# Optimization experiments

Hardware: AMD Instinct MI355X
Metric: run time of the kernel (lower is better)

The kernel has to match this reference:

```python
import jax, jax.numpy as jnp
import numpy as np

B, S, D = 4, 512, 256

def setup_inputs() -> dict:
    key = jax.random.key(0)
    ks = jax.random.split(key, 32)
    def w(k, shape, s=0.05):
        return jax.random.normal(k, shape, dtype=jnp.float32) * s
    inp = {
        "img": jax.random.normal(ks[0], (B, S, D), dtype=jnp.float32),
        "audio": jax.random.normal(ks[1], (B, S, D), dtype=jnp.float32),
        "common": jax.random.normal(ks[2], (B, S, D), dtype=jnp.float32),
    }
    names = ["qv", "qa", "kv", "ka", "cc", "w5", "w6", "w7", "w8"]
    for i, n in enumerate(names):
        inp[n + "_w"] = w(ks[3 + 2 * i], (D, D))   # stored [in, out]
        inp[n + "_b"] = w(ks[4 + 2 * i], (D,))
    inp["bil_w"] = w(ks[25], (D, D, D))            # Bilinear weight [out, in1, in2]
    inp["t_o"] = jnp.ones((), dtype=jnp.float32)
    return inp


def reference(img, audio, common,
              qv_w, qv_b, qa_w, qa_b, kv_w, kv_b, ka_w, ka_b, cc_w, cc_b,
              w5_w, w5_b, w6_w, w6_b, w7_w, w7_b, w8_w, w8_b,
              bil_w, t_o):
    dim_k = qv_w.shape[1]
    norm_fact = 1.0 / jnp.sqrt(jnp.asarray(dim_k, dtype=jnp.float32))

    lin = lambda x, w, b: x @ w + b
    # NOTE: faithful to source - softmax first, THEN scaled by norm_fact.
    attn = lambda q, k: jax.nn.softmax(jnp.einsum('bsd,btd->bst', q, k), axis=-1) * norm_fact

    W_q_v = lin(img, qv_w, qv_b)
    W_q_a = lin(audio, qa_w, qa_b)
    w_k_a = lin(audio, ka_w, ka_b)
    W_k_v = lin(img, kv_w, kv_b)
    C_c = lin(common, cc_w, cc_b)

    atten_vv = attn(W_q_v, W_k_v)
    atten_vc = attn(W_q_v, C_c)
    atten_aa = attn(W_q_a, w_k_a)
    atten_ac = attn(W_q_a, C_c)

    vc_common = jnp.einsum('bst,btd->bsd', atten_vc, common)
    ac_common = jnp.einsum('bst,btd->bsd', atten_ac, common)

    common_feat_v = (1.0 + lin(vc_common, w5_w, w5_b)) * jnp.einsum('bst,btd->bsd', atten_vv, img) + lin(vc_common, w6_w, w6_b)
    common_feat_a = (1.0 + lin(ac_common, w7_w, w7_b)) * jnp.einsum('bst,btd->bsd', atten_aa, audio) + lin(ac_common, w8_w, w8_b)

    # Bilinear: out[b,s,k] = v[b,s,:] @ W[k] @ a[b,s,:]
    atten_m = jnp.einsum('bsi,kij,bsj->bsk', common_feat_v, bil_w, common_feat_a)
    j_o = jax.nn.sigmoid(atten_m)
    Z_k_o = t_o * j_o * img + (1.0 - j_o) * audio
    return (Z_k_o + img, Z_k_o + audio)
```

## Files before the change

### kernel.cpp

```cpp
#include <hip/hip_runtime.h>
#include <hip/hip_bf16.h>

typedef unsigned short ushortT;
typedef __bf16 bf16x8 __attribute__((ext_vector_type(8)));
typedef float f32x4 __attribute__((ext_vector_type(4)));
typedef ushortT ush8 __attribute__((ext_vector_type(8)));
typedef ushortT ush4 __attribute__((ext_vector_type(4)));

#define MFMA16(a, b, c) __builtin_amdgcn_mfma_f32_16x16x32_bf16((a), (b), (c), 0, 0, 0)

__device__ __forceinline__ ushortT f2b(float f) {
  __hip_bfloat16 h = __float2bfloat16(f);
  return __builtin_bit_cast(ushortT, h);
}
__device__ __forceinline__ float b2f(ushortT u) {
  __hip_bfloat16 h = __builtin_bit_cast(__hip_bfloat16, u);
  return __bfloat162float(h);
}

__device__ __forceinline__ void async16(const void* g, void* l) {
  __builtin_amdgcn_global_load_lds((const __attribute__((address_space(1))) unsigned int*)g,
                                   (__attribute__((address_space(3))) unsigned int*)l, 16, 0, 0);
}

#define ACT_E 524288
#define WD_E  65536

#define OFF_ACT16   0u
#define OFF_ACTT16  3145728u
#define OFF_W16T    6291456u
#define OFF_PROJ16  7471104u
#define OFF_P16     12713984u
#define OFF_VC16    21102592u
#define OFF_AC16    22151168u
#define OFF_PVV32   23199744u
#define OFF_PVA32   25296896u
#define OFF_PART    0u
#define OFF_BIL16   33554432u
#define OFF_CFV16   67108864u
#define OFF_CFA16   68157440u

__global__ void k_cvt_acts(const float* __restrict__ img, const float* __restrict__ aud,
                           const float* __restrict__ com, ushortT* __restrict__ dst) {
  int i4 = blockIdx.x * 256 + threadIdx.x;
#pragma unroll
  for (int q = 0; q < 4; q++) {
    int idx4 = i4 + q * 98304;
    int flat = idx4 * 4;
    const float* src;
    int off;
    if (flat < 524288)        { src = img; off = flat; }
    else if (flat < 1048576)  { src = aud; off = flat - 524288; }
    else                      { src = com; off = flat - 1048576; }
    float4 v = *(const float4*)(src + off);
    ush4 u = { f2b(v.x), f2b(v.y), f2b(v.z), f2b(v.w) };
    *(ush4*)(dst + idx4 * 4) = u;
  }
}

__global__ void k_cvt_bil(const float* __restrict__ bil, ushortT* __restrict__ dst) {
  int i4 = blockIdx.x * 256 + threadIdx.x;
#pragma unroll
  for (int q = 0; q < 8; q++) {
    int idx4 = i4 + q * 524288;
    float4 v = *(const float4*)(bil + idx4 * 4);
    ush4 u = { f2b(v.x), f2b(v.y), f2b(v.z), f2b(v.w) };
    *(ush4*)(dst + idx4 * 4) = u;
  }
}

__global__ void k_transpose(const float* __restrict__ img, const float* __restrict__ aud,
                            const float* __restrict__ com,
                            const float* w0, const float* w1, const float* w2,
                            const float* w3, const float* w4, const float* w5,
                            const float* w6, const float* w7, const float* w8,
                            ushortT* __restrict__ actT, ushortT* __restrict__ wT) {
  __shared__ ushortT tl[64][72];
  int tid = threadIdx.x;
  int bx = blockIdx.x;
  const float* src;
  ushortT* dst;
  int R, C, r0, c0;
  if (bx < 384) {
    int inst = bx >> 5, tile = bx & 31;
    int act = inst >> 2, bb = inst & 3;
    src = (act == 0 ? img : (act == 1 ? aud : com)) + bb * 131072;
    dst = actT + act * 524288 + bb * 131072;
    R = 512; C = 256;
    r0 = (tile >> 2) * 64; c0 = (tile & 3) * 64;
  } else {
    int bw = bx - 384;
    int w = bw >> 4, tile = bw & 15;
    const float* s;
    switch (w) {
      case 0: s = w0; break; case 1: s = w1; break; case 2: s = w2; break;
      case 3: s = w3; break; case 4: s = w4; break; case 5: s = w5; break;
      case 6: s = w6; break; case 7: s = w7; break; default: s = w8; break;
    }
    src = s;
    dst = wT + w * 65536;
    R = 256; C = 256;
    r0 = (tile >> 2) * 64; c0 = (tile & 3) * 64;
  }
#pragma unroll
  for (int q = 0; q < 4; q++) {
    int rr = q * 16 + (tid >> 4);
    int cs = (tid & 15) * 4;
    float4 v = *(const float4*)(src + (r0 + rr) * C + c0 + cs);
    tl[rr][cs + 0] = f2b(v.x);
    tl[rr][cs + 1] = f2b(v.y);
    tl[rr][cs + 2] = f2b(v.z);
    tl[rr][cs + 3] = f2b(v.w);
  }
  __syncthreads();
#pragma unroll
  for (int q = 0; q < 4; q++) {
    int cc = q * 16 + (tid >> 4);
    int rs = (tid & 15) * 4;
    ush4 u = { tl[rs + 0][cc], tl[rs + 1][cc], tl[rs + 2][cc], tl[rs + 3][cc] };
    *(ush4*)(dst + (c0 + cc) * R + r0 + rs) = u;
  }
}

__global__ __launch_bounds__(512) void k_linear5(
    const ushortT* __restrict__ act16, const ushortT* __restrict__ wT,
    const float* __restrict__ b0, const float* __restrict__ b1,
    const float* __restrict__ b2, const float* __restrict__ b3,
    const float* __restrict__ b4, ushortT* __restrict__ proj16) {
  __shared__ ushortT Al[4][32][8];
  __shared__ ushortT Bl[4][256][8];
  const int tid = threadIdx.x, l = tid & 63, w = tid >> 6;
  const int bx = blockIdx.x;
  const int op = bx >> 6, sblk = bx & 63;
  const int s0 = sblk * 32;
  const int xsel = (op == 4) ? 2 : (op & 1);
  const ushortT* X = act16 + xsel * ACT_E;
  const ushortT* W = wT + op * WD_E;
  const float* bias = op == 0 ? b0 : op == 1 ? b1 : op == 2 ? b2 : op == 3 ? b3 : b4;
  ushortT* out = proj16 + op * ACT_E;

  f32x4 acc[2][2] = {};
  ush8 ra, rb[2];
  int a_row = tid >> 2, a_seg = tid & 3;

  auto sload = [&](int k0) {
    if (tid < 128) ra = *(const ush8*)(X + (s0 + a_row) * 256 + k0 + a_seg * 8);
#pragma unroll
    for (int q = 0; q < 2; q++) {
      int slot = tid + q * 512;
      rb[q] = *(const ush8*)(W + (slot >> 2) * 256 + k0 + (slot & 3) * 8);
    }
  };
  auto swrite = [&]() {
    if (tid < 128) *(ush8*)(&Al[a_seg][a_row][0]) = ra;
#pragma unroll
    for (int q = 0; q < 2; q++) {
      int slot = tid + q * 512;
      *(ush8*)(&Bl[slot & 3][slot >> 2][0]) = rb[q];
    }
  };

  sload(0); swrite(); __syncthreads();
  for (int s = 0; s < 8; s++) {
    if (s < 7) sload((s + 1) * 32);
    int ks = l >> 4;
    bf16x8 a[2], bb[2];
#pragma unroll
    for (int m = 0; m < 2; m++) a[m] = *(const bf16x8*)(&Al[ks][m * 16 + (l & 15)][0]);
#pragma unroll
    for (int n = 0; n < 2; n++) bb[n] = *(const bf16x8*)(&Bl[ks][w * 32 + n * 16 + (l & 15)][0]);
#pragma unroll
    for (int m = 0; m < 2; m++)
#pragma unroll
      for (int n = 0; n < 2; n++) acc[m][n] = MFMA16(a[m], bb[n], acc[m][n]);
    if (s == 7) break;
    __syncthreads();
    swrite();
    __syncthreads();
  }
#pragma unroll
  for (int m = 0; m < 2; m++)
#pragma unroll
    for (int n = 0; n < 2; n++)
#pragma unroll
      for (int r = 0; r < 4; r++) {
        int row = s0 + m * 16 + (l >> 4) * 4 + r;
        int col = w * 32 + n * 16 + (l & 15);
        out[row * 256 + col] = f2b(acc[m][n][r] + bias[col]);
      }
}

__global__ __launch_bounds__(512) void k_attn(const ushortT* __restrict__ proj16,
                                              ushortT* __restrict__ P16) {
  __shared__ ushortT Ql[8][4][32][8];
  __shared__ ushortT Kl[4][512][8];
  __shared__ float red[32][8];
  const int tid = threadIdx.x, l = tid & 63, w = tid >> 6;
  const int bx = blockIdx.x;
  const int p = bx >> 6, b = (bx >> 4) & 3, sblk = bx & 15;
  const int s0 = sblk * 32;
  const int qsel = (p < 2) ? 0 : 1;
  const int ksel = (p == 0) ? 2 : (p == 2) ? 3 : 4;
  const ushortT* Q = proj16 + qsel * ACT_E + b * 131072;
  const ushortT* K = proj16 + ksel * ACT_E + b * 131072;
  ushortT* P = P16 + p * 1048576 + b * 262144;

#pragma unroll
  for (int q = 0; q < 2; q++) {
    int slot = tid + q * 512;
    int row = slot >> 5, seg = slot & 31;
    ush8 v = *(const ush8*)(Q + (s0 + row) * 256 + seg * 8);
    *(ush8*)(&Ql[seg >> 2][seg & 3][row][0]) = v;
  }

  f32x4 acc[2][4] = {};
  ush8 rk[4];
  auto kload = [&](int d0) {
#pragma unroll
    for (int q = 0; q < 4; q++) {
      int slot = tid + q * 512;
      rk[q] = *(const ush8*)(K + (slot >> 2) * 256 + d0 + (slot & 3) * 8);
    }
  };
  auto kwrite = [&]() {
#pragma unroll
    for (int q = 0; q < 4; q++) {
      int slot = tid + q * 512;
      *(ush8*)(&Kl[slot & 3][slot >> 2][0]) = rk[q];
    }
  };

  kload(0); kwrite(); __syncthreads();
  for (int s = 0; s < 8; s++) {
    if (s < 7) kload((s + 1) * 32);
    int ks = l >> 4;
    bf16x8 a[2], bb[4];
#pragma unroll
    for (int m = 0; m < 2; m++) a[m] = *(const bf16x8*)(&Ql[s][ks][m * 16 + (l & 15)][0]);
#pragma unroll
    for (int n = 0; n < 4; n++) bb[n] = *(const bf16x8*)(&Kl[ks][w * 64 + n * 16 + (l & 15)][0]);
#pragma unroll
    for (int m = 0; m < 2; m++)
#pragma unroll
      for (int n = 0; n < 4; n++) acc[m][n] = MFMA16(a[m], bb[n], acc[m][n]);
    if (s == 7) break;
    __syncthreads();
    kwrite();
    __syncthreads();
  }

  float gmax[2][4];
#pragma unroll
  for (int m = 0; m < 2; m++)
#pragma unroll
    for (int r = 0; r < 4; r++) {
      float v = fmaxf(fmaxf(acc[m][0][r], acc[m][1][r]), fmaxf(acc[m][2][r], acc[m][3][r]));
#pragma unroll
      for (int off = 1; off < 16; off <<= 1) v = fmaxf(v, __shfl_xor(v, off, 16));
      if ((l & 15) == 0) red[m * 16 + (l >> 4) * 4 + r][w] = v;
    }
  __syncthreads();
#pragma unroll
  for (int m = 0; m < 2; m++)
#pragma unroll
    for (int r = 0; r < 4; r++) {
      int sr = m * 16 + (l >> 4) * 4 + r;
      float g = red[sr][0];
#pragma unroll
      for (int ww = 1; ww < 8; ww++) g = fmaxf(g, red[sr][ww]);
      gmax[m][r] = g;
    }
  __syncthreads();
#pragma unroll
  for (int m = 0; m < 2; m++)
#pragma unroll
    for (int r = 0; r < 4; r++) {
      float ssum = 0.f;
#pragma unroll
      for (int n = 0; n < 4; n++) {
        float e = __expf(acc[m][n][r] - gmax[m][r]);
        acc[m][n][r] = e;
        ssum += e;
      }
#pragma unroll
      for (int off = 1; off < 16; off <<= 1) ssum += __shfl_xor(ssum, off, 16);
      if ((l & 15) == 0) red[m * 16 + (l >> 4) * 4 + r][w] = ssum;
    }
  __syncthreads();
#pragma unroll
  for (int m = 0; m < 2; m++)
#pragma unroll
    for (int r = 0; r < 4; r++) {
      int sr = m * 16 + (l >> 4) * 4 + r;
      float tot = 0.f;
#pragma unroll
      for (int ww = 0; ww < 8; ww++) tot += red[sr][ww];
      float sc = 0.0625f / tot;
#pragma unroll
      for (int n = 0; n < 4; n++)
        P[(s0 + sr) * 512 + w * 64 + n * 16 + (l & 15)] = f2b(acc[m][n][r] * sc);
    }
}

__global__ __launch_bounds__(512) void k_pv(const ushortT* __restrict__ P16,
                                            const ushortT* __restrict__ actT,
                                            float* __restrict__ pvv, float* __restrict__ pva,
                                            ushortT* __restrict__ vc16, ushortT* __restrict__ ac16) {
  __shared__ ushortT Al[4][32][8];
  __shared__ ushortT Bl[4][256][8];
  const int tid = threadIdx.x, l = tid & 63, w = tid >> 6;
  const int bx = blockIdx.x;
  const int p = bx >> 6, b = (bx >> 4) & 3, sblk = bx & 15;
  const int s0 = sblk * 32;
  const ushortT* A = P16 + p * 1048576 + b * 262144;
  const int vsel = (p == 0) ? 0 : (p == 2) ? 1 : 2;
  const ushortT* VT = actT + vsel * ACT_E + b * 131072;

  f32x4 acc[2][2] = {};
  ush8 ra, rb[2];
  int a_row = tid >> 2, a_seg = tid & 3;
  auto sload = [&](int t0) {
    if (tid < 128) ra = *(const ush8*)(A + (s0 + a_row) * 512 + t0 + a_seg * 8);
#pragma unroll
    for (int q = 0; q < 2; q++) {
      int slot = tid + q * 512;
      rb[q] = *(const ush8*)(VT + (slot >> 2) * 512 + t0 + (slot & 3) * 8);
    }
  };
  auto swrite = [&]() {
    if (tid < 128) *(ush8*)(&Al[a_seg][a_row][0]) = ra;
#pragma unroll
    for (int q = 0; q < 2; q++) {
      int slot = tid + q * 512;
      *(ush8*)(&Bl[slot & 3][slot >> 2][0]) = rb[q];
    }
  };

  sload(0); swrite(); __syncthreads();
  for (int s = 0; s < 16; s++) {
    if (s < 15) sload((s + 1) * 32);
    int ks = l >> 4;
    bf16x8 a[2], bb[2];
#pragma unroll
    for (int m = 0; m < 2; m++) a[m] = *(const bf16x8*)(&Al[ks][m * 16 + (l & 15)][0]);
#pragma unroll
    for (int n = 0; n < 2; n++) bb[n] = *(const bf16x8*)(&Bl[ks][w * 32 + n * 16 + (l & 15)][0]);
#pragma unroll
    for (int m = 0; m < 2; m++)
#pragma unroll
      for (int n = 0; n < 2; n++) acc[m][n] = MFMA16(a[m], bb[n], acc[m][n]);
    if (s == 15) break;
    __syncthreads();
    swrite();
    __syncthreads();
  }
#pragma unroll
  for (int m = 0; m < 2; m++)
#pragma unroll
    for (int n = 0; n < 2; n++)
#pragma unroll
      for (int r = 0; r < 4; r++) {
        int row = s0 + m * 16 + (l >> 4) * 4 + r;
        int col = w * 32 + n * 16 + (l & 15);
        int gi = (b * 512 + row) * 256 + col;
        float v = acc[m][n][r];
        if (p == 0) pvv[gi] = v;
        else if (p == 1) vc16[gi] = f2b(v);
        else if (p == 2) pva[gi] = v;
        else ac16[gi] = f2b(v);
      }
}

__global__ __launch_bounds__(512) void k_lin4c(
    const ushortT* __restrict__ vc16, const ushortT* __restrict__ ac16,
    const ushortT* __restrict__ wT,
    const float* __restrict__ w5b, const float* __restrict__ w6b,
    const float* __restrict__ w7b, const float* __restrict__ w8b,
    const float* __restrict__ pvv, const float* __restrict__ pva,
    ushortT* __restrict__ cfv, ushortT* __restrict__ cfa) {
  __shared__ ushortT Al[4][32][8];
  __shared__ ushortT B1[4][256][8];
  __shared__ ushortT B2[4][256][8];
  const int tid = threadIdx.x, l = tid & 63, w = tid >> 6;
  const int bx = blockIdx.x;
  const int side = bx >> 6, sblk = bx & 63;
  const int s0 = sblk * 32;
  const ushortT* A = side ? ac16 : vc16;
  const ushortT* W1 = wT + (side ? 7 : 5) * WD_E;
  const ushortT* W2 = wT + (side ? 8 : 6) * WD_E;
  const float* bb1 = side ? w7b : w5b;
  const float* bb2 = side ? w8b : w6b;
  const float* pv = side ? pva : pvv;
  ushortT* out = side ? cfa : cfv;

  f32x4 acc1[2][2] = {}, acc2[2][2] = {};
  ush8 ra, rb1[2], rb2[2];
  int a_row = tid >> 2, a_seg = tid & 3;
  auto sload = [&](int k0) {
    if (tid < 128) ra = *(const ush8*)(A + (s0 + a_row) * 256 + k0 + a_seg * 8);
#pragma unroll
    for (int q = 0; q < 2; q++) {
      int slot = tid + q * 512;
      rb1[q] = *(const ush8*)(W1 + (slot >> 2) * 256 + k0 + (slot & 3) * 8);
      rb2[q] = *(const ush8*)(W2 + (slot >> 2) * 256 + k0 + (slot & 3) * 8);
    }
  };
  auto swrite = [&]() {
    if (tid < 128) *(ush8*)(&Al[a_seg][a_row][0]) = ra;
#pragma unroll
    for (int q = 0; q < 2; q++) {
      int slot = tid + q * 512;
      *(ush8*)(&B1[slot & 3][slot >> 2][0]) = rb1[q];
      *(ush8*)(&B2[slot & 3][slot >> 2][0]) = rb2[q];
    }
  };

  sload(0); swrite(); __syncthreads();
  for (int s = 0; s < 8; s++) {
    if (s < 7) sload((s + 1) * 32);
    int ks = l >> 4;
    bf16x8 a[2], x1[2], x2[2];
#pragma unroll
    for (int m = 0; m < 2; m++) a[m] = *(const bf16x8*)(&Al[ks][m * 16 + (l & 15)][0]);
#pragma unroll
    for (int n = 0; n < 2; n++) {
      x1[n] = *(const bf16x8*)(&B1[ks][w * 32 + n * 16 + (l & 15)][0]);
      x2[n] = *(const bf16x8*)(&B2[ks][w * 32 + n * 16 + (l & 15)][0]);
    }
#pragma unroll
    for (int m = 0; m < 2; m++)
#pragma unroll
      for (int n = 0; n < 2; n++) {
        acc1[m][n] = MFMA16(a[m], x1[n], acc1[m][n]);
        acc2[m][n] = MFMA16(a[m], x2[n], acc2[m][n]);
      }
    if (s == 7) break;
    __syncthreads();
    swrite();
    __syncthreads();
  }
#pragma unroll
  for (int m = 0; m < 2; m++)
#pragma unroll
    for (int n = 0; n < 2; n++)
#pragma unroll
      for (int r = 0; r < 4; r++) {
        int row = s0 + m * 16 + (l >> 4) * 4 + r;
        int col = w * 32 + n * 16 + (l & 15);
        int gi = row * 256 + col;
        float u1 = acc1[m][n][r] + bb1[col];
        float u2 = acc2[m][n][r] + bb2[col];
        out[gi] = f2b((1.f + u1) * pv[gi] + u2);
      }
}

__global__ __launch_bounds__(256, 2) void k_bilinear4(
    const ushortT* __restrict__ cfa, const ushortT* __restrict__ cfv,
    const ushortT* __restrict__ W, float* __restrict__ part) {
  __shared__ char arena[73728];
  const int tid = threadIdx.x, l = tid & 63, w = tid >> 6;
  const int d = blockIdx.x;
  const int L = (d & 7) * 64 + (d >> 3);
  const int ic = L >> 5;
  const int nb = (L >> 4) & 1;
  const int mb = L & 15;
  const int r0 = mb * 128;
  const int ko0 = nb * 128;
  const int wr = w >> 1, wc = w & 1;

  float* cfvl = (float*)(arena + 65536);
  {
    int row = tid >> 1, seg = tid & 1;
    ush8 v = *(const ush8*)(cfv + (r0 + row) * 256 + ic * 16 + seg * 8);
    float* dptr = cfvl + row * 16 + seg * 8;
#pragma unroll
    for (int q = 0; q < 8; q++) dptr[q] = b2f(v[q]);
  }
  __syncthreads();

  const char* gA[4];
  const char* gB[4];
#pragma unroll
  for (int s = 0; s < 4; s++) {
    int p = (tid + s * 256) * 16;
    int lg = p ^ (((p >> 7) & 7) << 4);
    int row = lg >> 7, colb = lg & 127;
    gA[s] = (const char*)cfa + (size_t)(r0 + row) * 512 + colb;
    gB[s] = (const char*)W + (size_t)(ko0 + row) * 131072 + (size_t)ic * 8192 + colb;
  }

  int aoff0[4], aoff1[4], boff0[4], boff1[4];
#pragma unroll
  for (int m = 0; m < 4; m++) {
    int row = wr * 64 + m * 16 + (l & 15);
    int b0 = row * 128 + (l >> 4) * 16;
    int msk = (row & 7) << 4;
    aoff0[m] = b0 ^ msk;
    aoff1[m] = (b0 + 64) ^ msk;
  }
#pragma unroll
  for (int n = 0; n < 4; n++) {
    int row = wc * 64 + n * 16 + (l & 15);
    int b0 = row * 128 + (l >> 4) * 16;
    int msk = (row & 7) << 4;
    boff0[n] = b0 ^ msk;
    boff1[n] = (b0 + 64) ^ msk;
  }

  f32x4 macc[4][4] = {};
  f32x4 acci[4][4] = {};

  auto stage = [&](int t, char* bufbase) {
    int ja = (t & 3) << 7;
    int jb = t << 7;
#pragma unroll
    for (int s = 0; s < 4; s++)
      async16(gA[s] + ja, bufbase + (tid + s * 256) * 16);
#pragma unroll
    for (int s = 0; s < 4; s++)
      async16(gB[s] + jb, bufbase + 16384 + (tid + s * 256) * 16);
  };

  stage(0, arena);

  int buf = 0;
  for (int t = 0; t < 64; t++) {
    asm volatile("s_waitcnt vmcnt(0)" ::: "memory");
    __builtin_amdgcn_s_barrier();

    char* Ab = arena + buf * 32768;
    char* Bb = Ab + 16384;

    bf16x8 a0[4], b0v[4];
#pragma unroll
    for (int m = 0; m < 4; m++) a0[m] = *(const bf16x8*)(Ab + aoff0[m]);
#pragma unroll
    for (int n = 0; n < 4; n++) b0v[n] = *(const bf16x8*)(Bb + boff0[n]);

    if (t < 63) stage(t + 1, arena + (buf ^ 1) * 32768);

    __builtin_amdgcn_s_setprio(1);
#pragma unroll
    for (int m = 0; m < 4; m++)
#pragma unroll
      for (int n = 0; n < 4; n++) acci[m][n] = MFMA16(a0[m], b0v[n], acci[m][n]);
    __builtin_amdgcn_s_setprio(0);

    bf16x8 a1[4], b1v[4];
#pragma unroll
    for (int m = 0; m < 4; m++) a1[m] = *(const bf16x8*)(Ab + aoff1[m]);
#pragma unroll
    for (int n = 0; n < 4; n++) b1v[n] = *(const bf16x8*)(Bb + boff1[n]);

    __builtin_amdgcn_s_setprio(1);
#pragma unroll
    for (int m = 0; m < 4; m++)
#pragma unroll
      for (int n = 0; n < 4; n++) acci[m][n] = MFMA16(a1[m], b1v[n], acci[m][n]);
    __builtin_amdgcn_s_setprio(0);

    if ((t & 3) == 3) {
      int il = t >> 2;
#pragma unroll
      for (int m = 0; m < 4; m++) {
        int rbase = wr * 64 + m * 16 + ((l >> 4) << 2);
        float c0 = cfvl[(rbase + 0) * 16 + il];
        float c1 = cfvl[(rbase + 1) * 16 + il];
        float c2 = cfvl[(rbase + 2) * 16 + il];
        float c3 = cfvl[(rbase + 3) * 16 + il];
#pragma unroll
        for (int n = 0; n < 4; n++) {
          macc[m][n][0] += c0 * acci[m][n][0];
          macc[m][n][1] += c1 * acci[m][n][1];
          macc[m][n][2] += c2 * acci[m][n][2];
          macc[m][n][3] += c3 * acci[m][n][3];
          acci[m][n] = (f32x4){0.f, 0.f, 0.f, 0.f};
        }
      }
    }
    buf ^= 1;
  }

  float* dst = part + (size_t)ic * 524288 + (size_t)r0 * 256 + ko0;
#pragma unroll
  for (int m = 0; m < 4; m++)
#pragma unroll
    for (int n = 0; n < 4; n++)
#pragma unroll
      for (int r = 0; r < 4; r++)
        dst[(wr * 64 + m * 16 + ((l >> 4) << 2) + r) * 256 + wc * 64 + n * 16 + (l & 15)] =
            macc[m][n][r];
}

__global__ void k_final2(const float* __restrict__ part, const float* __restrict__ img,
                         const float* __restrict__ aud, const float* __restrict__ t_o,
                         float* __restrict__ out0, float* __restrict__ out1) {
  int i = blockIdx.x * 256 + threadIdx.x;
  float t = t_o[0];
  float4 m = {0.f, 0.f, 0.f, 0.f};
#pragma unroll
  for (int ic = 0; ic < 16; ic++) {
    float4 p = ((const float4*)(part + ic * 524288))[i];
    m.x += p.x; m.y += p.y; m.z += p.z; m.w += p.w;
  }
  float4 a = ((const float4*)img)[i];
  float4 u = ((const float4*)aud)[i];
  float4 o0, o1;
  {
    float j = 1.f / (1.f + __expf(-m.x)); float Z = t * j * a.x + (1.f - j) * u.x;
    o0.x = Z + a.x; o1.x = Z + u.x;
  }
  {
    float j = 1.f / (1.f + __expf(-m.y)); float Z = t * j * a.y + (1.f - j) * u.y;
    o0.y = Z + a.y; o1.y = Z + u.y;
  }
  {
    float j = 1.f / (1.f + __expf(-m.z)); float Z = t * j * a.z + (1.f - j) * u.z;
    o0.z = Z + a.z; o1.z = Z + u.z;
  }
  {
    float j = 1.f / (1.f + __expf(-m.w)); float Z = t * j * a.w + (1.f - j) * u.w;
    o0.w = Z + a.w; o1.w = Z + u.w;
  }
  ((float4*)out0)[i] = o0;
  ((float4*)out1)[i] = o1;
}

extern "C" void kernel_launch(void* const* d_in, const int* in_sizes, int n_in,
                              void* d_out, int out_size, void* d_ws, size_t ws_size,
                              hipStream_t stream) {
  const float* img   = (const float*)d_in[0];
  const float* aud   = (const float*)d_in[1];
  const float* com   = (const float*)d_in[2];
  const float* qv_w  = (const float*)d_in[3];
  const float* qv_b  = (const float*)d_in[4];
  const float* qa_w  = (const float*)d_in[5];
  const float* qa_b  = (const float*)d_in[6];
  const float* kv_w  = (const float*)d_in[7];
  const float* kv_b  = (const float*)d_in[8];
  const float* ka_w  = (const float*)d_in[9];
  const float* ka_b  = (const float*)d_in[10];
  const float* cc_w  = (const float*)d_in[11];
  const float* cc_b  = (const float*)d_in[12];
  const float* w5_w  = (const float*)d_in[13];
  const float* w5_b  = (const float*)d_in[14];
  const float* w6_w  = (const float*)d_in[15];
  const float* w6_b  = (const float*)d_in[16];
  const float* w7_w  = (const float*)d_in[17];
  const float* w7_b  = (const float*)d_in[18];
  const float* w8_w  = (const float*)d_in[19];
  const float* w8_b  = (const float*)d_in[20];
  const float* bil_w = (const float*)d_in[21];
  const float* t_o   = (const float*)d_in[22];
  float* out = (float*)d_out;

  char* ws = (char*)d_ws;
  ushortT* act16  = (ushortT*)(ws + OFF_ACT16);
  ushortT* actT16 = (ushortT*)(ws + OFF_ACTT16);
  ushortT* w16t   = (ushortT*)(ws + OFF_W16T);
  ushortT* proj16 = (ushortT*)(ws + OFF_PROJ16);
  ushortT* P16    = (ushortT*)(ws + OFF_P16);
  ushortT* vc16   = (ushortT*)(ws + OFF_VC16);
  ushortT* ac16   = (ushortT*)(ws + OFF_AC16);
  float*   pvv32  = (float*)(ws + OFF_PVV32);
  float*   pva32  = (float*)(ws + OFF_PVA32);
  float*   part   = (float*)(ws + OFF_PART);
  ushortT* bil16  = (ushortT*)(ws + OFF_BIL16);
  ushortT* cfv16  = (ushortT*)(ws + OFF_CFV16);
  ushortT* cfa16  = (ushortT*)(ws + OFF_CFA16);

  k_cvt_acts<<<384, 256, 0, stream>>>(img, aud, com, act16);
  k_cvt_bil<<<2048, 256, 0, stream>>>(bil_w, bil16);
  k_transpose<<<528, 256, 0, stream>>>(img, aud, com, qv_w, qa_w, kv_w, ka_w, cc_w,
                                       w5_w, w6_w, w7_w, w8_w, actT16, w16t);
  k_linear5<<<320, 512, 0, stream>>>(act16, w16t, qv_b, qa_b, kv_b, ka_b, cc_b, proj16);
  k_attn<<<256, 512, 0, stream>>>(proj16, P16);
  k_pv<<<256, 512, 0, stream>>>(P16, actT16, pvv32, pva32, vc16, ac16);
  k_lin4c<<<128, 512, 0, stream>>>(vc16, ac16, w16t, w5_b, w6_b, w7_b, w8_b,
                                   pvv32, pva32, cfv16, cfa16);
  k_bilinear4<<<512, 256, 0, stream>>>(cfa16, cfv16, bil16, part);
  k_final2<<<512, 256, 0, stream>>>(part, img, aud, t_o, out, out + 524288);
}
```

Before: 153.3 us.

## Enlarge bilinear block tile to 256 rows and triple-buffer the async loads

The bilinear kernel now runs 512-thread blocks that each cover 256 output rows instead of 128. Each block therefore shares one bilinear-weight tile across twice as many rows, which halves the number of times the weight tensor is re-read from the cache hierarchy. The LDS pipeline moves from double to triple buffering with a two-stage-ahead prefetch and a partial vmcnt wait, so loads overlap more of the MFMA work. The cfv coefficients are now kept as bf16 in LDS and converted when used. The trade-off is that the roughly 152 KB of LDS allows only one block per CU, and the grid shrinks to 256 blocks.

```diff
diff --git a/kernel.cpp b/kernel.cpp
--- a/kernel.cpp
+++ b/kernel.cpp
@@ -454,91 +454,91 @@
       }
 }
 
-__global__ __launch_bounds__(256, 2) void k_bilinear4(
+__global__ __launch_bounds__(512, 2) void k_bilinear5(
     const ushortT* __restrict__ cfa, const ushortT* __restrict__ cfv,
     const ushortT* __restrict__ W, float* __restrict__ part) {
-  __shared__ char arena[73728];
+  __shared__ char arena[155648];
   const int tid = threadIdx.x, l = tid & 63, w = tid >> 6;
   const int d = blockIdx.x;
-  const int L = (d & 7) * 64 + (d >> 3);
-  const int ic = L >> 5;
-  const int nb = (L >> 4) & 1;
-  const int mb = L & 15;
-  const int r0 = mb * 128;
+  const int L = (d & 7) * 32 + (d >> 3);
+  const int ic = L >> 4;
+  const int mb = (L >> 1) & 7;
+  const int nb = L & 1;
+  const int r0 = mb * 256;
   const int ko0 = nb * 128;
   const int wr = w >> 1, wc = w & 1;
 
-  float* cfvl = (float*)(arena + 65536);
+  ushortT* cfvl = (ushortT*)(arena + 147456);
   {
     int row = tid >> 1, seg = tid & 1;
-    ush8 v = *(const ush8*)(cfv + (r0 + row) * 256 + ic * 16 + seg * 8);
-    float* dptr = cfvl + row * 16 + seg * 8;
-#pragma unroll
-    for (int q = 0; q < 8; q++) dptr[q] = b2f(v[q]);
+    *(ush8*)(cfvl + row * 16 + seg * 8) =
+        *(const ush8*)(cfv + (r0 + row) * 256 + ic * 16 + seg * 8);
   }
   __syncthreads();
 
   const char* gA[4];
-  const char* gB[4];
+  const char* gB[2];
 #pragma unroll
   for (int s = 0; s < 4; s++) {
-    int p = (tid + s * 256) * 16;
+    int p = (tid + s * 512) * 16;
     int lg = p ^ (((p >> 7) & 7) << 4);
-    int row = lg >> 7, colb = lg & 127;
-    gA[s] = (const char*)cfa + (size_t)(r0 + row) * 512 + colb;
-    gB[s] = (const char*)W + (size_t)(ko0 + row) * 131072 + (size_t)ic * 8192 + colb;
-  }
-
-  int aoff0[4], aoff1[4], boff0[4], boff1[4];
+    gA[s] = (const char*)cfa + (size_t)(r0 + (lg >> 7)) * 512 + (lg & 127);
+  }
+#pragma unroll
+  for (int s = 0; s < 2; s++) {
+    int p = (tid + s * 512) * 16;
+    int lg = p ^ (((p >> 7) & 7) << 4);
+    gB[s] = (const char*)W + (size_t)(ko0 + (lg >> 7)) * 131072 + (size_t)ic * 8192 + (lg & 127);
+  }
+
+  auto stage = [&](int t) {
+    char* Ab = arena + (t % 3) * 32768;
+    char* Bb = arena + 98304 + (t % 3) * 16384;
+    int ja = (t & 3) << 7;
+    int jb = t << 7;
+#pragma unroll
+    for (int s = 0; s < 4; s++) async16(gA[s] + ja, Ab + (tid + s * 512) * 16);
+#pragma unroll
+    for (int s = 0; s < 2; s++) async16(gB[s] + jb, Bb + (tid + s * 512) * 16);
+  };
+
+  int aoff[2][4], boff[2][4];
 #pragma unroll
   for (int m = 0; m < 4; m++) {
     int row = wr * 64 + m * 16 + (l & 15);
     int b0 = row * 128 + (l >> 4) * 16;
     int msk = (row & 7) << 4;
-    aoff0[m] = b0 ^ msk;
-    aoff1[m] = (b0 + 64) ^ msk;
+    aoff[0][m] = b0 ^ msk;
+    aoff[1][m] = (b0 + 64) ^ msk;
   }
 #pragma unroll
   for (int n = 0; n < 4; n++) {
     int row = wc * 64 + n * 16 + (l & 15);
     int b0 = row * 128 + (l >> 4) * 16;
     int msk = (row & 7) << 4;
-    boff0[n] = b0 ^ msk;
-    boff1[n] = (b0 + 64) ^ msk;
+    boff[0][n] = b0 ^ msk;
+    boff[1][n] = (b0 + 64) ^ msk;
   }
 
   f32x4 macc[4][4] = {};
   f32x4 acci[4][4] = {};
 
-  auto stage = [&](int t, char* bufbase) {
-    int ja = (t & 3) << 7;
-    int jb = t << 7;
-#pragma unroll
-    for (int s = 0; s < 4; s++)
-      async16(gA[s] + ja, bufbase + (tid + s * 256) * 16);
-#pragma unroll
-    for (int s = 0; s < 4; s++)
-      async16(gB[s] + jb, bufbase + 16384 + (tid + s * 256) * 16);
-  };
-
-  stage(0, arena);
-
-  int buf = 0;
+  stage(0);
+  stage(1);
+
   for (int t = 0; t < 64; t++) {
-    asm volatile("s_waitcnt vmcnt(0)" ::: "memory");
+    if (t < 62) asm volatile("s_waitcnt vmcnt(6)" ::: "memory");
+    else        asm volatile("s_waitcnt vmcnt(0)" ::: "memory");
     __builtin_amdgcn_s_barrier();
 
-    char* Ab = arena + buf * 32768;
-    char* Bb = Ab + 16384;
+    char* Ab = arena + (t % 3) * 32768;
+    char* Bb = arena + 98304 + (t % 3) * 16384;
 
     bf16x8 a0[4], b0v[4];
 #pragma unroll
-    for (int m = 0; m < 4; m++) a0[m] = *(const bf16x8*)(Ab + aoff0[m]);
-#pragma unroll
-    for (int n = 0; n < 4; n++) b0v[n] = *(const bf16x8*)(Bb + boff0[n]);
-
-    if (t < 63) stage(t + 1, arena + (buf ^ 1) * 32768);
-
+    for (int m = 0; m < 4; m++) a0[m] = *(const bf16x8*)(Ab + aoff[0][m]);
+#pragma unroll
+    for (int n = 0; n < 4; n++) b0v[n] = *(const bf16x8*)(Bb + boff[0][n]);
     __builtin_amdgcn_s_setprio(1);
 #pragma unroll
     for (int m = 0; m < 4; m++)
@@ -546,12 +546,13 @@
       for (int n = 0; n < 4; n++) acci[m][n] = MFMA16(a0[m], b0v[n], acci[m][n]);
     __builtin_amdgcn_s_setprio(0);
 
+    if (t + 2 < 64) stage(t + 2);
+
     bf16x8 a1[4], b1v[4];
 #pragma unroll
-    for (int m = 0; m < 4; m++) a1[m] = *(const bf16x8*)(Ab + aoff1[m]);
-#pragma unroll
-    for (int n = 0; n < 4; n++) b1v[n] = *(const bf16x8*)(Bb + boff1[n]);
-
+    for (int m = 0; m < 4; m++) a1[m] = *(const bf16x8*)(Ab + aoff[1][m]);
+#pragma unroll
+    for (int n = 0; n < 4; n++) b1v[n] = *(const bf16x8*)(Bb + boff[1][n]);
     __builtin_amdgcn_s_setprio(1);
 #pragma unroll
     for (int m = 0; m < 4; m++)
@@ -564,10 +565,10 @@
 #pragma unroll
       for (int m = 0; m < 4; m++) {
         int rbase = wr * 64 + m * 16 + ((l >> 4) << 2);
-        float c0 = cfvl[(rbase + 0) * 16 + il];
-        float c1 = cfvl[(rbase + 1) * 16 + il];
-        float c2 = cfvl[(rbase + 2) * 16 + il];
-        float c3 = cfvl[(rbase + 3) * 16 + il];
+        float c0 = b2f(cfvl[(rbase + 0) * 16 + il]);
+        float c1 = b2f(cfvl[(rbase + 1) * 16 + il]);
+        float c2 = b2f(cfvl[(rbase + 2) * 16 + il]);
+        float c3 = b2f(cfvl[(rbase + 3) * 16 + il]);
 #pragma unroll
         for (int n = 0; n < 4; n++) {
           macc[m][n][0] += c0 * acci[m][n][0];
@@ -578,7 +579,6 @@
         }
       }
     }
-    buf ^= 1;
   }
 
   float* dst = part + (size_t)ic * 524288 + (size_t)r0 * 256 + ko0;
@@ -678,6 +678,6 @@
   k_pv<<<256, 512, 0, stream>>>(P16, actT16, pvv32, pva32, vc16, ac16);
   k_lin4c<<<128, 512, 0, stream>>>(vc16, ac16, w16t, w5_b, w6_b, w7_b, w8_b,
                                    pvv32, pva32, cfv16, cfa16);
-  k_bilinear4<<<512, 256, 0, stream>>>(cfa16, cfv16, bil16, part);
+  k_bilinear5<<<256, 512, 0, stream>>>(cfa16, cfv16, bil16, part);
   k_final2<<<512, 256, 0, stream>>>(part, img, aud, t_o, out, out + 524288);
 }
```

Result: no change. 150.8 us (-1.6%).
